# Optimization experiments

Measured on AMD Instinct MI355X. Metric: run time of the kernel, lower is better.

## Reference

```python
import jax, jax.numpy as jnp
import numpy as np
import math

G = 256      # graphs per batch
N0 = 256     # nodes per graph at input
RATIO = 0.5  # TopKPooling ratio


def gcn_conv(x, src, dst, ew, W, b):
    h = x @ W
    n = x.shape[0]
    deg = jnp.zeros((n,), x.dtype).at[dst].add(ew) + 1.0  # +1 for self-loop
    dinv = jax.lax.rsqrt(deg)
    norm = dinv[src] * dinv[dst] * ew
    agg = jnp.zeros_like(h).at[dst].add(norm[:, None] * h[src])
    return agg + h / deg[:, None] + b  # self-loop norm = 1/deg


def topk_pool(x, src, dst, ew, w, n_per_graph):
    # PyG TopKPooling: score = tanh(x.w/||w||); keep top ceil(ratio*n) per graph;
    # x_out = x[perm] * score[perm]; edges between dropped nodes are masked out.
    k = int(math.ceil(RATIO * n_per_graph))
    score = jnp.tanh((x @ w) / jnp.linalg.norm(w))
    top_s, top_i = jax.lax.top_k(score.reshape(G, n_per_graph), k)  # [G,k]
    perm = (top_i + (jnp.arange(G) * n_per_graph)[:, None]).reshape(-1)
    new_x = x[perm] * top_s.reshape(-1, 1)
    new_id = jnp.full((x.shape[0],), -1, jnp.int32).at[perm].set(
        jnp.arange(G * k, dtype=jnp.int32))
    ns, nd = new_id[src], new_id[dst]
    valid = (ns >= 0) & (nd >= 0)
    new_ew = ew * valid.astype(x.dtype)
    ns = jnp.where(valid, ns, 0)
    nd = jnp.where(valid, nd, 0)
    new_batch = jnp.repeat(jnp.arange(G, dtype=jnp.int32), k)
    return new_x, ns, nd, new_ew, new_batch, k


def readout(x, batch):
    # torch.cat([global_max_pool, global_mean_pool], dim=1)
    mx = jax.ops.segment_max(x, batch, num_segments=G)
    cnt = jax.ops.segment_sum(jnp.ones((x.shape[0],), x.dtype), batch, num_segments=G)
    mn = jax.ops.segment_sum(x, batch, num_segments=G) / cnt[:, None]
    return jnp.concatenate([mx, mn], axis=1)


def _forward(x, edge_index, batch, gcn_w0, gcn_b0, gcn_w1, gcn_b1, gcn_w2, gcn_b2,
             pool_w0, pool_w1, pool_w2, lin1_w, lin1_b, lin2_w, lin2_b, lin3_w, lin3_b):
    src, dst = edge_index[0], edge_index[1]
    ew = jnp.ones((src.shape[0],), x.dtype)
    npg = N0
    h = jax.nn.relu(gcn_conv(x, src, dst, ew, gcn_w0, gcn_b0))
    h, src, dst, ew, batch, npg = topk_pool(h, src, dst, ew, pool_w0, npg)
    out = readout(h, batch)
    for Wg, bg, pw in ((gcn_w1, gcn_b1, pool_w1), (gcn_w2, gcn_b2, pool_w2)):
        h = jax.nn.relu(gcn_conv(h, src, dst, ew, Wg, bg))
        h, src, dst, ew, batch, npg = topk_pool(h, src, dst, ew, pw, npg)
        out = out + readout(h, batch)
    h1 = jax.nn.relu(out @ lin1_w + lin1_b)  # dropout = identity (eval mode)
    h2 = jax.nn.relu(h1 @ lin2_w + lin2_b)
    logits = h2 @ lin3_w + lin3_b
    return jax.nn.log_softmax(logits, axis=-1)


def setup_inputs() -> dict:
    key = jax.random.key(0)
    ks = jax.random.split(key, 16)
    EPG = 2048  # edges per graph (avg degree 8)
    F_IN, H = 128, 256
    num_nodes, E = G * N0, G * EPG
    x = jax.random.normal(ks[0], (num_nodes, F_IN), jnp.float32)
    offs = jnp.repeat(jnp.arange(G, dtype=jnp.int32) * N0, EPG)
    src = offs + jax.random.randint(ks[1], (E,), 0, N0, dtype=jnp.int32)
    dst = offs + jax.random.randint(ks[2], (E,), 0, N0, dtype=jnp.int32)

    def glorot(k, shape):
        lim = float(np.sqrt(6.0 / (shape[0] + shape[1])))
        return jax.random.uniform(k, shape, jnp.float32, -lim, lim)

    return {
        "x": x,
        "edge_index": jnp.stack([src, dst]),
        "batch": jnp.arange(num_nodes, dtype=jnp.int32) // N0,
        "gcn_w0": glorot(ks[3], (F_IN, H)), "gcn_b0": jnp.zeros((H,), jnp.float32),
        "gcn_w1": glorot(ks[4], (H, H)), "gcn_b1": jnp.zeros((H,), jnp.float32),
        "gcn_w2": glorot(ks[5], (H, H)), "gcn_b2": jnp.zeros((H,), jnp.float32),
        "pool_w0": jax.random.normal(ks[6], (H,), jnp.float32) * 0.1,
        "pool_w1": jax.random.normal(ks[7], (H,), jnp.float32) * 0.1,
        "pool_w2": jax.random.normal(ks[8], (H,), jnp.float32) * 0.1,
        "lin1_w": glorot(ks[9], (2 * H, H)), "lin1_b": jnp.zeros((H,), jnp.float32),
        "lin2_w": glorot(ks[10], (H, H // 2)), "lin2_b": jnp.zeros((H // 2,), jnp.float32),
        "lin3_w": glorot(ks[11], (H // 2, 2)), "lin3_b": jnp.zeros((2,), jnp.float32),
    }


def reference(x, edge_index, batch, gcn_w0, gcn_b0, gcn_w1, gcn_b1, gcn_w2, gcn_b2,
              pool_w0, pool_w1, pool_w2, lin1_w, lin1_b, lin2_w, lin2_b, lin3_w, lin3_b):
    return _forward(x, edge_index, batch, gcn_w0, gcn_b0, gcn_w1, gcn_b1, gcn_w2, gcn_b2,
                    pool_w0, pool_w1, pool_w2, lin1_w, lin1_b, lin2_w, lin2_b, lin3_w, lin3_b)
```

## Files before the change

kernel.cpp:

```cpp
#include <hip/hip_runtime.h>
#include <hip/hip_bf16.h>
#include <math.h>

#define G_GRAPHS 256
#define EPG 2048
#define E_TOT 524288
#define HF 256
#define FIN 128

__global__ void init_cur(int* __restrict__ cur) {
    int i = blockIdx.x * blockDim.x + threadIdx.x;
    if (i < G_GRAPHS * 256) cur[i] = i & 255;
}

template <int K>
__global__ __launch_bounds__(256, 4)
void gemm_v8(const float* __restrict__ A, const float* __restrict__ W,
             float* __restrict__ C) {
    __shared__ __align__(16) float As[32 * 68];
    __shared__ __align__(16) float Wa[32 * 68];
    __shared__ __align__(16) float Wb[32 * 68];
    const int tid = threadIdx.x;
    const int tx = tid & 15;
    const int ty = tid >> 4;
    const int r0 = blockIdx.x * 64;
    const int c0 = blockIdx.y * 128;
    const int l8 = tid >> 3;
    const int kq = tid & 7;
    const int wkk = tid >> 5;
    const int wc = tid & 31;
    float acc[4][8] = {{0.f}};
    float4 va0, va1, vw0, vw1, vw2, vw3;

    auto load_regs = [&](int k0) {
        va0 = *(const float4*)&A[(size_t)(r0 + l8) * K + k0 + 4 * kq];
        va1 = *(const float4*)&A[(size_t)(r0 + 32 + l8) * K + k0 + 4 * kq];
        vw0 = *(const float4*)&W[(size_t)(k0 + 0  + wkk) * 256 + c0 + 4 * wc];
        vw1 = *(const float4*)&W[(size_t)(k0 + 8  + wkk) * 256 + c0 + 4 * wc];
        vw2 = *(const float4*)&W[(size_t)(k0 + 16 + wkk) * 256 + c0 + 4 * wc];
        vw3 = *(const float4*)&W[(size_t)(k0 + 24 + wkk) * 256 + c0 + 4 * wc];
    };
    auto write_stage = [&]() {
        {
            int rs = l8 ^ (kq << 3);
            As[(4 * kq + 0) * 68 + rs] = va0.x;
            As[(4 * kq + 1) * 68 + rs] = va0.y;
            As[(4 * kq + 2) * 68 + rs] = va0.z;
            As[(4 * kq + 3) * 68 + rs] = va0.w;
        }
        {
            int rs = (32 + l8) ^ (kq << 3);
            As[(4 * kq + 0) * 68 + rs] = va1.x;
            As[(4 * kq + 1) * 68 + rs] = va1.y;
            As[(4 * kq + 2) * 68 + rs] = va1.z;
            As[(4 * kq + 3) * 68 + rs] = va1.w;
        }
        if (wc < 16) {
            *(float4*)&Wa[(0  + wkk) * 68 + 4 * wc] = vw0;
            *(float4*)&Wa[(8  + wkk) * 68 + 4 * wc] = vw1;
            *(float4*)&Wa[(16 + wkk) * 68 + 4 * wc] = vw2;
            *(float4*)&Wa[(24 + wkk) * 68 + 4 * wc] = vw3;
        } else {
            *(float4*)&Wb[(0  + wkk) * 68 + 4 * (wc - 16)] = vw0;
            *(float4*)&Wb[(8  + wkk) * 68 + 4 * (wc - 16)] = vw1;
            *(float4*)&Wb[(16 + wkk) * 68 + 4 * (wc - 16)] = vw2;
            *(float4*)&Wb[(24 + wkk) * 68 + 4 * (wc - 16)] = vw3;
        }
    };
    auto compute = [&]() {
#pragma unroll 4
        for (int kk = 0; kk < 32; ++kk) {
            const int g = (ty * 4) ^ ((kk >> 2) << 3);
            const float4 a0 = *(const float4*)&As[kk * 68 + g];
            const float4 w0 = *(const float4*)&Wa[kk * 68 + tx * 4];
            const float4 w1 = *(const float4*)&Wb[kk * 68 + tx * 4];
            float av[4] = {a0.x, a0.y, a0.z, a0.w};
            float wv_[8] = {w0.x, w0.y, w0.z, w0.w, w1.x, w1.y, w1.z, w1.w};
#pragma unroll
            for (int i = 0; i < 4; ++i)
#pragma unroll
                for (int j = 0; j < 8; ++j)
                    acc[i][j] += av[i] * wv_[j];
        }
    };

    load_regs(0);
    write_stage();
    __syncthreads();
    for (int k0 = 0; k0 < K - 32; k0 += 32) {
        load_regs(k0 + 32);
        compute();
        __syncthreads();
        write_stage();
        __syncthreads();
    }
    compute();

#pragma unroll
    for (int i = 0; i < 4; ++i) {
        float4 v0 = make_float4(acc[i][0], acc[i][1], acc[i][2], acc[i][3]);
        float4 v1 = make_float4(acc[i][4], acc[i][5], acc[i][6], acc[i][7]);
        size_t base = (size_t)(r0 + ty * 4 + i) * 256 + c0 + tx * 4;
        *(float4*)&C[base] = v0;
        *(float4*)&C[base + 64] = v1;
    }
}

__global__ __launch_bounds__(256)
void csr_build(const int* __restrict__ ei, const int* __restrict__ cur, int npg,
               int* __restrict__ degS, float* __restrict__ dinvS,
               int* __restrict__ startsS, int2* __restrict__ slots2) {
    __shared__ int cul[EPG];
    __shared__ short dstv[EPG];
    __shared__ unsigned char rnk[EPG];
    __shared__ int h[32][256];
    __shared__ int cnt[256];
    __shared__ int st[256];
    const int g = blockIdx.x;
    const int t = threadIdx.x;
    const int lane = t & 63;
    const int wv = t >> 6;

    for (int i = t; i < 32 * 256; i += 256) ((int*)h)[i] = 0;
    for (int e = t; e < EPG; e += 256) {
        size_t idx = (size_t)g * EPG + e;
        int cu = cur[g * 256 + (ei[idx] - g * 256)];
        int cv = cur[g * 256 + (ei[E_TOT + idx] - g * 256)];
        bool valid = (cu >= 0 && cv >= 0);
        cul[e] = cu;
        dstv[e] = valid ? (short)cv : (short)256;
    }
    __syncthreads();
    for (int c = wv; c < 32; c += 4) {
        int e = c * 64 + lane;
        int d = (int)dstv[e];
        unsigned long long m = ~0ULL;
#pragma unroll
        for (int b = 0; b < 9; ++b) {
            unsigned long long bb = __ballot((d >> b) & 1);
            m &= ((d >> b) & 1) ? bb : ~bb;
        }
        int r = __popcll(m & ((1ULL << lane) - 1ULL));
        rnk[e] = (unsigned char)r;
        if (r == 0 && d < 256) h[c][d] = __popcll(m);
    }
    __syncthreads();
    if (t < npg) {
        int run = 0;
        for (int c = 0; c < 32; ++c) { int v = h[c][t]; h[c][t] = run; run += v; }
        cnt[t] = run;
        degS[g * npg + t] = run + 1;
        dinvS[g * npg + t] = 1.0f / sqrtf((float)(run + 1));
    }
    __syncthreads();
    if (t == 0) {
        int run = 0;
        for (int i = 0; i < npg; ++i) { st[i] = run; run += cnt[i]; }
    }
    __syncthreads();
    if (t < npg) startsS[g * npg + t] = g * EPG + st[t];
    for (int e = t; e < EPG; e += 256) {
        int d = (int)dstv[e];
        if (d < npg) {
            int slot = st[d] + h[e >> 6][d] + (int)rnk[e];
            int cu = cul[e];
            float dv = 1.0f / sqrtf((float)(cnt[cu] + 1));
            slots2[g * EPG + slot] = make_int2(g * npg + cu, __float_as_int(dv));
        }
    }
}

__global__ __launch_bounds__(256)
void agg_score2(const int* __restrict__ degS, const float* __restrict__ dinvS,
                const int* __restrict__ startsS, const int2* __restrict__ slots2,
                const float* __restrict__ HL, float* __restrict__ H2,
                const float* __restrict__ bias, const float* __restrict__ pw,
                float* __restrict__ score, int nbOver8) {
    __shared__ float vrow[4][256];
    const int t = threadIdx.x;
    const int wv = t >> 6;
    const int lane = t & 63;
    const int blk = (blockIdx.x & 7) * nbOver8 + (blockIdx.x >> 3);
    const int node = blk * 4 + wv;
    const int cntE = degS[node] - 1;
    const float degF = (float)(cntE + 1);
    const float dn = dinvS[node];
    const int2* sl = slots2 + startsS[node];
    float ax = 0.f, ay = 0.f, az = 0.f, aw = 0.f;
    int j = 0;
    for (; j + 8 <= cntE; j += 8) {
        int2 s[8];
#pragma unroll
        for (int u = 0; u < 8; ++u) s[u] = sl[j + u];
        float4 hv[8];
#pragma unroll
        for (int u = 0; u < 8; ++u)
            hv[u] = *(const float4*)&HL[(size_t)s[u].x * 256 + 4 * lane];
#pragma unroll
        for (int u = 0; u < 8; ++u) {
            float dv = __int_as_float(s[u].y);
            ax += dv * hv[u].x; ay += dv * hv[u].y;
            az += dv * hv[u].z; aw += dv * hv[u].w;
        }
    }
    for (; j + 4 <= cntE; j += 4) {
        int2 s[4];
#pragma unroll
        for (int u = 0; u < 4; ++u) s[u] = sl[j + u];
        float4 hv[4];
#pragma unroll
        for (int u = 0; u < 4; ++u)
            hv[u] = *(const float4*)&HL[(size_t)s[u].x * 256 + 4 * lane];
#pragma unroll
        for (int u = 0; u < 4; ++u) {
            float dv = __int_as_float(s[u].y);
            ax += dv * hv[u].x; ay += dv * hv[u].y;
            az += dv * hv[u].z; aw += dv * hv[u].w;
        }
    }
    for (; j < cntE; ++j) {
        int2 sv = sl[j];
        float dv = __int_as_float(sv.y);
        float4 hv = *(const float4*)&HL[(size_t)sv.x * 256 + 4 * lane];
        ax += dv * hv.x; ay += dv * hv.y; az += dv * hv.z; aw += dv * hv.w;
    }
    const float4 hn = *(const float4*)&HL[(size_t)node * 256 + 4 * lane];
    const float4 bi = *(const float4*)&bias[4 * lane];
    float4 v;
    v.x = ax * dn + hn.x / degF + bi.x;  v.x = fmaxf(v.x, 0.f);
    v.y = ay * dn + hn.y / degF + bi.y;  v.y = fmaxf(v.y, 0.f);
    v.z = az * dn + hn.z / degF + bi.z;  v.z = fmaxf(v.z, 0.f);
    v.w = aw * dn + hn.w / degF + bi.w;  v.w = fmaxf(v.w, 0.f);
    *(float4*)&H2[(size_t)node * 256 + 4 * lane] = v;
    *(float4*)&vrow[wv][4 * lane] = v;
    float pr = 0.f, s2p = 0.f;
    for (int jj = 0; jj < 4; ++jj) {
        int f = lane + 64 * jj;
        float w = pw[f];
        pr += vrow[wv][f] * w;
        s2p += w * w;
    }
    for (int off = 32; off; off >>= 1) {
        pr += __shfl_down(pr, off, 64);
        s2p += __shfl_down(s2p, off, 64);
    }
    s2p = __shfl(s2p, 0, 64);
    if (lane == 0) score[node] = tanhf(pr / sqrtf(s2p));
}

__global__ __launch_bounds__(256)
void topk_fused(const float* __restrict__ score, int npg, int k,
                const float* __restrict__ H2, float* __restrict__ OUT,
                float* __restrict__ outacc, int* __restrict__ cur, int first) {
    __shared__ float ss[256];
    __shared__ int si_[256];
    __shared__ int rankOf[256];
    const int g = blockIdx.x;
    const int t = threadIdx.x;
    if (t < npg) { ss[t] = score[g * npg + t]; si_[t] = t; }
    else         { ss[t] = -INFINITY; si_[t] = 0x7FFFFFFF; }
    for (int size = 2; size <= 256; size <<= 1) {
        for (int stride = size >> 1; stride > 0; stride >>= 1) {
            __syncthreads();
            int i = t, j = t ^ stride;
            if (j > i) {
                float a = ss[i], b = ss[j];
                int ia = si_[i], ib = si_[j];
                bool inOrder = (a > b) || (a == b && ia < ib);
                bool desc = ((i & size) == 0);
                if (desc ? !inOrder : inOrder) {
                    ss[i] = b; ss[j] = a; si_[i] = ib; si_[j] = ia;
                }
            }
        }
    }
    __syncthreads();
    rankOf[t] = -1;
    __syncthreads();
    if (t < k) rankOf[si_[t]] = t;
    __syncthreads();
    {
        int v = g * 256 + t;
        int c = cur[v];
        cur[v] = (c >= 0) ? rankOf[c] : -1;
    }
    const size_t gb = (size_t)g * npg * 256;
    float mx = -INFINITY, sm = 0.f;
    for (int n = 0; n < k; n += 4) {
        float v0 = H2[gb + (size_t)si_[n + 0] * 256 + t] * ss[n + 0];
        float v1 = H2[gb + (size_t)si_[n + 1] * 256 + t] * ss[n + 1];
        float v2 = H2[gb + (size_t)si_[n + 2] * 256 + t] * ss[n + 2];
        float v3 = H2[gb + (size_t)si_[n + 3] * 256 + t] * ss[n + 3];
        size_t ob = ((size_t)g * k + n) * 256 + t;
        OUT[ob]       = v0;
        OUT[ob + 256] = v1;
        OUT[ob + 512] = v2;
        OUT[ob + 768] = v3;
        mx = fmaxf(mx, v0); sm += v0;
        mx = fmaxf(mx, v1); sm += v1;
        mx = fmaxf(mx, v2); sm += v2;
        mx = fmaxf(mx, v3); sm += v3;
    }
    float mean = sm / (float)k;
    if (first) {
        outacc[g * 512 + t] = mx;
        outacc[g * 512 + 256 + t] = mean;
    } else {
        outacc[g * 512 + t] += mx;
        outacc[g * 512 + 256 + t] += mean;
    }
}

__global__ __launch_bounds__(256)
void mlp_head(const float* __restrict__ outacc,
              const float* __restrict__ l1w, const float* __restrict__ l1b,
              const float* __restrict__ l2w, const float* __restrict__ l2b,
              const float* __restrict__ l3w, const float* __restrict__ l3b,
              float* __restrict__ out) {
    __shared__ float row[512];
    __shared__ float h1[256];
    __shared__ float h2[128];
    const int g = blockIdx.x;
    const int t = threadIdx.x;
    row[t] = outacc[g * 512 + t];
    row[256 + t] = outacc[g * 512 + 256 + t];
    __syncthreads();
    {
        float a = l1b[t];
        for (int j = 0; j < 512; ++j) a += row[j] * l1w[j * 256 + t];
        h1[t] = fmaxf(a, 0.f);
    }
    __syncthreads();
    if (t < 128) {
        float a2 = l2b[t];
        for (int j = 0; j < 256; ++j) a2 += h1[j] * l2w[j * 128 + t];
        h2[t] = fmaxf(a2, 0.f);
    }
    __syncthreads();
    if (t == 0) {
        float l0 = l3b[0], l1 = l3b[1];
        for (int j = 0; j < 128; ++j) {
            float h = h2[j];
            l0 += h * l3w[j * 2 + 0];
            l1 += h * l3w[j * 2 + 1];
        }
        float m = fmaxf(l0, l1);
        float lse = m + logf(expf(l0 - m) + expf(l1 - m));
        out[g * 2 + 0] = l0 - lse;
        out[g * 2 + 1] = l1 - lse;
    }
}

__global__ __launch_bounds__(256, 1)
void gnn_mono(const float* __restrict__ x, const int* __restrict__ ei,
              const float* __restrict__ gw0, const float* __restrict__ gb0,
              const float* __restrict__ gw1, const float* __restrict__ gb1,
              const float* __restrict__ gw2, const float* __restrict__ gb2,
              const float* __restrict__ pw0, const float* __restrict__ pw1,
              const float* __restrict__ pw2,
              const float* __restrict__ l1w, const float* __restrict__ l1b,
              const float* __restrict__ l2w, const float* __restrict__ l2b,
              const float* __restrict__ l3w, const float* __restrict__ l3b,
              float* __restrict__ out, float* __restrict__ ws) {
    const int g = blockIdx.x;
    const int t = threadIdx.x;
    float* P = ws + (size_t)g * HF * 256;
    float* Q = ws + (size_t)G_GRAPHS * HF * 256 + (size_t)g * HF * 256;
    __shared__ int   eb[EPG];
    __shared__ int   slots[EPG];
    __shared__ int   curID[256];
    __shared__ int   cntL[256];
    __shared__ int   startL[256];
    __shared__ float degF[256];
    __shared__ float dinv[256];
    __shared__ float sa[256];
    __shared__ float ss[256];
    __shared__ int   si_[256];
    __shared__ float scoreV[256];
    __shared__ int   kept[128];
    __shared__ int   rankOf[256];
    __shared__ float row[512];
    for (int e = t; e < EPG; e += 256) {
        size_t idx = (size_t)g * EPG + e;
        eb[e] = ((ei[idx] - g * 256) << 8) | (ei[E_TOT + idx] - g * 256);
    }
    curID[t] = t;
    float accMx = 0.f, accMn = 0.f;
    const float* GW[3] = {gw0, gw1, gw2};
    const float* GB[3] = {gb0, gb1, gb2};
    const float* PW[3] = {pw0, pw1, pw2};
    const int kk[3] = {128, 64, 32};
    int npg = 256;
    __syncthreads();
    for (int s = 0; s < 3; ++s) {
        const int knext = kk[s];
        {
            const float* Wp = GW[s];
            const int K = (s == 0) ? FIN : HF;
            for (int n = 0; n < npg; ++n) {
                if (s == 0) { if (t < FIN) sa[t] = x[(size_t)(g * 256 + n) * FIN + t]; }
                else sa[t] = P[(size_t)n * HF + t];
                __syncthreads();
                float a = 0.f;
                for (int k2 = 0; k2 < K; ++k2) a += sa[k2] * Wp[k2 * HF + t];
                Q[(size_t)n * HF + t] = a;
                __syncthreads();
            }
        }
        cntL[t] = 0;
        __syncthreads();
        for (int e = t; e < EPG; e += 256) {
            int p = eb[e];
            int cu = curID[p >> 8], cv = curID[p & 255];
            if (cu >= 0 && cv >= 0) atomicAdd(&cntL[cv], 1);
        }
        __syncthreads();
        if (t == 0) { int run = 0; for (int i = 0; i < npg; ++i) { startL[i] = run; run += cntL[i]; } }
        __syncthreads();
        if (t < npg) {
            float d = (float)cntL[t] + 1.0f;
            degF[t] = d;
            dinv[t] = 1.0f / sqrtf(d);
            int c = startL[t];
            for (int e = 0; e < EPG; ++e) {
                int p = eb[e];
                int cu = curID[p >> 8], cv = curID[p & 255];
                if (cu >= 0 && cv >= 0 && cv == t) slots[c++] = e;
            }
        }
        __syncthreads();
        {
            const float bb = GB[s][t];
            for (int n = 0; n < npg; ++n) {
                float acc = 0.f;
                const int s0 = startL[n], s1 = s0 + cntL[n];
                for (int j = s0; j < s1; ++j) {
                    int scur = curID[eb[slots[j]] >> 8];
                    acc += dinv[scur] * Q[(size_t)scur * HF + t];
                }
                float v = acc * dinv[n] + Q[(size_t)n * HF + t] / degF[n] + bb;
                P[(size_t)n * HF + t] = fmaxf(v, 0.f);
            }
        }
        __syncthreads();
        {
            const float* pwp = PW[s];
            const int lane = t & 63, wv = t >> 6;
            float s2p = 0.f;
            for (int j = 0; j < 4; ++j) { float w = pwp[lane + 64 * j]; s2p += w * w; }
            for (int off = 32; off; off >>= 1) s2p += __shfl_down(s2p, off, 64);
            s2p = __shfl(s2p, 0, 64);
            const float nw = sqrtf(s2p);
            for (int n = wv; n < npg; n += 4) {
                float pr = 0.f;
                for (int j = 0; j < 4; ++j) { int f = lane + 64 * j; pr += P[(size_t)n * HF + f] * pwp[f]; }
                for (int off = 32; off; off >>= 1) pr += __shfl_down(pr, off, 64);
                if (lane == 0) scoreV[n] = tanhf(pr / nw);
            }
        }
        __syncthreads();
        if (t < npg) { ss[t] = scoreV[t]; si_[t] = t; }
        else         { ss[t] = -INFINITY; si_[t] = 0x7FFFFFFF; }
        for (int size = 2; size <= 256; size <<= 1) {
            for (int stride = size >> 1; stride > 0; stride >>= 1) {
                __syncthreads();
                int i = t, j = t ^ stride;
                if (j > i) {
                    float a = ss[i], b = ss[j];
                    int ia = si_[i], ib = si_[j];
                    bool inOrder = (a > b) || (a == b && ia < ib);
                    bool desc = ((i & size) == 0);
                    if (desc ? !inOrder : inOrder) { ss[i] = b; ss[j] = a; si_[i] = ib; si_[j] = ia; }
                }
            }
        }
        __syncthreads();
        if (t < knext) kept[t] = si_[t];
        __syncthreads();
        {
            float mx = -INFINITY, sm = 0.f;
            for (int n = 0; n < knext; ++n) {
                int o = kept[n];
                float vv = P[(size_t)o * HF + t] * scoreV[o];
                Q[(size_t)n * HF + t] = vv;
                mx = fmaxf(mx, vv);
                sm += vv;
            }
            accMx += mx;
            accMn += sm / (float)knext;
        }
        rankOf[t] = -1;
        __syncthreads();
        if (t < knext) rankOf[kept[t]] = t;
        __syncthreads();
        { int c = curID[t]; curID[t] = (c >= 0) ? rankOf[c] : -1; }
        __syncthreads();
        { float* tmp = P; P = Q; Q = tmp; }
        npg = knext;
    }
    row[t] = accMx;
    row[256 + t] = accMn;
    __syncthreads();
    { float a = l1b[t]; for (int j = 0; j < 512; ++j) a += row[j] * l1w[j * 256 + t]; scoreV[t] = fmaxf(a, 0.f); }
    __syncthreads();
    if (t < 128) { float a2 = l2b[t]; for (int j = 0; j < 256; ++j) a2 += scoreV[j] * l2w[j * 128 + t]; sa[t] = fmaxf(a2, 0.f); }
    __syncthreads();
    if (t == 0) {
        float l0 = l3b[0], l1 = l3b[1];
        for (int j = 0; j < 128; ++j) { float h = sa[j]; l0 += h * l3w[j * 2 + 0]; l1 += h * l3w[j * 2 + 1]; }
        float m = fmaxf(l0, l1);
        float lse = m + logf(expf(l0 - m) + expf(l1 - m));
        out[g * 2 + 0] = l0 - lse;
        out[g * 2 + 1] = l1 - lse;
    }
}

extern "C" void kernel_launch(void* const* d_in, const int* in_sizes, int n_in,
                              void* d_out, int out_size, void* d_ws, size_t ws_size,
                              hipStream_t stream) {
    const float* x   = (const float*)d_in[0];
    const int*   ei  = (const int*)d_in[1];
    const float* gw0 = (const float*)d_in[3];
    const float* gb0 = (const float*)d_in[4];
    const float* gw1 = (const float*)d_in[5];
    const float* gb1 = (const float*)d_in[6];
    const float* gw2 = (const float*)d_in[7];
    const float* gb2 = (const float*)d_in[8];
    const float* pw0 = (const float*)d_in[9];
    const float* pw1 = (const float*)d_in[10];
    const float* pw2 = (const float*)d_in[11];
    const float* l1w = (const float*)d_in[12];
    const float* l1b = (const float*)d_in[13];
    const float* l2w = (const float*)d_in[14];
    const float* l2b = (const float*)d_in[15];
    const float* l3w = (const float*)d_in[16];
    const float* l3b = (const float*)d_in[17];
    float* out = (float*)d_out;

    const size_t SLAB = (size_t)65536 * 256;
    char* p = (char*)d_ws;
    float* P      = (float*)p; p += SLAB * 4;
    float* Q      = (float*)p; p += SLAB * 4;
    int*   cur    = (int*)p;   p += (size_t)65536 * 4;
    int*   degS   = (int*)p;   p += (size_t)65536 * 4;
    float* dinvS  = (float*)p; p += (size_t)65536 * 4;
    int*   starts = (int*)p;   p += (size_t)65536 * 4;
    int2*  slots2 = (int2*)p;  p += (size_t)E_TOT * 8;
    float* score  = (float*)p; p += (size_t)65536 * 4;
    int*   kept   = (int*)p;   p += (size_t)32768 * 4;
    float* outacc = (float*)p; p += (size_t)G_GRAPHS * 512 * 4;
    const size_t needed = (size_t)(p - (char*)d_ws);

    if (ws_size < needed) {
        gnn_mono<<<G_GRAPHS, 256, 0, stream>>>(
            x, ei, gw0, gb0, gw1, gb1, gw2, gb2, pw0, pw1, pw2,
            l1w, l1b, l2w, l2b, l3w, l3b, out, (float*)d_ws);
        return;
    }

    init_cur<<<(G_GRAPHS * 256 + 255) / 256, 256, 0, stream>>>(cur);

    const int   npg[3] = {256, 128, 64};
    const int   kk[3]  = {128, 64, 32};
    const int   Ns[3]  = {65536, 32768, 16384};
    const float* GW[3] = {gw0, gw1, gw2};
    const float* GB[3] = {gb0, gb1, gb2};
    const float* PW[3] = {pw0, pw1, pw2};

    float* HLs[3]   = {P, Q, P};
    float* H2s[3]   = {Q, P, Q};
    float* POOLs[3] = {P, Q, P};

    for (int s = 0; s < 3; ++s) {
        const int n = Ns[s];
        const int k = kk[s];
        if (s == 0) {
            gemm_v8<FIN><<<dim3(n / 64, 2), 256, 0, stream>>>(x, GW[s], HLs[s]);
        } else {
            gemm_v8<HF><<<dim3(n / 64, 2), 256, 0, stream>>>(POOLs[s - 1], GW[s], HLs[s]);
        }
        csr_build<<<G_GRAPHS, 256, 0, stream>>>(ei, cur, npg[s],
                                                degS, dinvS, starts, slots2);
        agg_score2<<<n / 4, 256, 0, stream>>>(degS, dinvS, starts, slots2,
                                              HLs[s], H2s[s], GB[s], PW[s], score,
                                              n / 32);
        topk_fused<<<G_GRAPHS, 256, 0, stream>>>(score, npg[s], k,
                                                 H2s[s], POOLs[s], outacc, cur,
                                                 s == 0 ? 1 : 0);
    }

    mlp_head<<<G_GRAPHS, 256, 0, stream>>>(outacc, l1w, l1b, l2w, l2b, l3w, l3b, out);
}
```

Baseline: 456.3 us.

## Fuse CSR build into topk and init kernels, fold final topk into MLP head

```diff
diff --git a/kernel.cpp b/kernel.cpp
--- a/kernel.cpp
+++ b/kernel.cpp
@@ -7,11 +7,6 @@
 #define E_TOT 524288
 #define HF 256
 #define FIN 128
-
-__global__ void init_cur(int* __restrict__ cur) {
-    int i = blockIdx.x * blockDim.x + threadIdx.x;
-    if (i < G_GRAPHS * 256) cur[i] = i & 255;
-}
 
 template <int K>
 __global__ __launch_bounds__(256, 4)
@@ -106,10 +101,70 @@
     }
 }
 
+template <bool IDENT>
+__device__ __forceinline__ void csr_body(
+    const int* __restrict__ ei, int g, int t, int npg, const int* curL,
+    int* __restrict__ degS, float* __restrict__ dinvS,
+    int* __restrict__ startsS, int2* __restrict__ slots2,
+    int* cul, short* dstv, unsigned char* rnk, int (*h)[256],
+    int* cnt, int* st) {
+    const int lane = t & 63;
+    const int wv = t >> 6;
+    for (int i = t; i < 32 * 256; i += 256) ((int*)h)[i] = 0;
+    for (int e = t; e < EPG; e += 256) {
+        size_t idx = (size_t)g * EPG + e;
+        int u = ei[idx] - g * 256;
+        int v = ei[E_TOT + idx] - g * 256;
+        int cu = IDENT ? u : curL[u];
+        int cv = IDENT ? v : curL[v];
+        bool valid = (cu >= 0 && cv >= 0);
+        cul[e] = cu;
+        dstv[e] = valid ? (short)cv : (short)256;
+    }
+    __syncthreads();
+    for (int c = wv; c < 32; c += 4) {
+        int e = c * 64 + lane;
+        int d = (int)dstv[e];
+        unsigned long long m = ~0ULL;
+#pragma unroll
+        for (int b = 0; b < 9; ++b) {
+            unsigned long long bb = __ballot((d >> b) & 1);
+            m &= ((d >> b) & 1) ? bb : ~bb;
+        }
+        int r = __popcll(m & ((1ULL << lane) - 1ULL));
+        rnk[e] = (unsigned char)r;
+        if (r == 0 && d < 256) h[c][d] = __popcll(m);
+    }
+    __syncthreads();
+    if (t < npg) {
+        int run = 0;
+        for (int c = 0; c < 32; ++c) { int v = h[c][t]; h[c][t] = run; run += v; }
+        cnt[t] = run;
+        degS[g * npg + t] = run + 1;
+        dinvS[g * npg + t] = 1.0f / sqrtf((float)(run + 1));
+    }
+    __syncthreads();
+    if (t == 0) {
+        int run = 0;
+        for (int i = 0; i < npg; ++i) { st[i] = run; run += cnt[i]; }
+    }
+    __syncthreads();
+    if (t < npg) startsS[g * npg + t] = g * EPG + st[t];
+    for (int e = t; e < EPG; e += 256) {
+        int d = (int)dstv[e];
+        if (d < npg) {
+            int slot = st[d] + h[e >> 6][d] + (int)rnk[e];
+            int cu = cul[e];
+            float dv = 1.0f / sqrtf((float)(cnt[cu] + 1));
+            slots2[g * EPG + slot] = make_int2(g * npg + cu, __float_as_int(dv));
+        }
+    }
+}
+
 __global__ __launch_bounds__(256)
-void csr_build(const int* __restrict__ ei, const int* __restrict__ cur, int npg,
-               int* __restrict__ degS, float* __restrict__ dinvS,
-               int* __restrict__ startsS, int2* __restrict__ slots2) {
+void fused_init_csr(const int* __restrict__ ei, int* __restrict__ cur,
+                    int* __restrict__ degS, float* __restrict__ dinvS,
+                    int* __restrict__ startsS, int2* __restrict__ slots2) {
     __shared__ int cul[EPG];
     __shared__ short dstv[EPG];
     __shared__ unsigned char rnk[EPG];
@@ -118,56 +173,9 @@
     __shared__ int st[256];
     const int g = blockIdx.x;
     const int t = threadIdx.x;
-    const int lane = t & 63;
-    const int wv = t >> 6;
-
-    for (int i = t; i < 32 * 256; i += 256) ((int*)h)[i] = 0;
-    for (int e = t; e < EPG; e += 256) {
-        size_t idx = (size_t)g * EPG + e;
-        int cu = cur[g * 256 + (ei[idx] - g * 256)];
-        int cv = cur[g * 256 + (ei[E_TOT + idx] - g * 256)];
-        bool valid = (cu >= 0 && cv >= 0);
-        cul[e] = cu;
-        dstv[e] = valid ? (short)cv : (short)256;
-    }
-    __syncthreads();
-    for (int c = wv; c < 32; c += 4) {
-        int e = c * 64 + lane;
-        int d = (int)dstv[e];
-        unsigned long long m = ~0ULL;
-#pragma unroll
-        for (int b = 0; b < 9; ++b) {
-            unsigned long long bb = __ballot((d >> b) & 1);
-            m &= ((d >> b) & 1) ? bb : ~bb;
-        }
-        int r = __popcll(m & ((1ULL << lane) - 1ULL));
-        rnk[e] = (unsigned char)r;
-        if (r == 0 && d < 256) h[c][d] = __popcll(m);
-    }
-    __syncthreads();
-    if (t < npg) {
-        int run = 0;
-        for (int c = 0; c < 32; ++c) { int v = h[c][t]; h[c][t] = run; run += v; }
-        cnt[t] = run;
-        degS[g * npg + t] = run + 1;
-        dinvS[g * npg + t] = 1.0f / sqrtf((float)(run + 1));
-    }
-    __syncthreads();
-    if (t == 0) {
-        int run = 0;
-        for (int i = 0; i < npg; ++i) { st[i] = run; run += cnt[i]; }
-    }
-    __syncthreads();
-    if (t < npg) startsS[g * npg + t] = g * EPG + st[t];
-    for (int e = t; e < EPG; e += 256) {
-        int d = (int)dstv[e];
-        if (d < npg) {
-            int slot = st[d] + h[e >> 6][d] + (int)rnk[e];
-            int cu = cul[e];
-            float dv = 1.0f / sqrtf((float)(cnt[cu] + 1));
-            slots2[g * EPG + slot] = make_int2(g * npg + cu, __float_as_int(dv));
-        }
-    }
+    cur[g * 256 + t] = t;
+    csr_body<true>(ei, g, t, 256, nullptr, degS, dinvS, startsS, slots2,
+                   cul, dstv, rnk, h, cnt, st);
 }
 
 __global__ __launch_bounds__(256)
@@ -249,12 +257,22 @@
 }
 
 __global__ __launch_bounds__(256)
-void topk_fused(const float* __restrict__ score, int npg, int k,
-                const float* __restrict__ H2, float* __restrict__ OUT,
-                float* __restrict__ outacc, int* __restrict__ cur, int first) {
+void fused_topk_csr(const float* __restrict__ score, int npg, int k,
+                    const float* __restrict__ H2, float* __restrict__ OUT,
+                    float* __restrict__ outacc, int* __restrict__ cur, int first,
+                    const int* __restrict__ ei,
+                    int* __restrict__ degS, float* __restrict__ dinvS,
+                    int* __restrict__ startsS, int2* __restrict__ slots2) {
     __shared__ float ss[256];
     __shared__ int si_[256];
     __shared__ int rankOf[256];
+    __shared__ int curL[256];
+    __shared__ int cul[EPG];
+    __shared__ short dstv[EPG];
+    __shared__ unsigned char rnk[EPG];
+    __shared__ int h[32][256];
+    __shared__ int cnt[256];
+    __shared__ int st[256];
     const int g = blockIdx.x;
     const int t = threadIdx.x;
     if (t < npg) { ss[t] = score[g * npg + t]; si_[t] = t; }
@@ -282,7 +300,9 @@
     {
         int v = g * 256 + t;
         int c = cur[v];
-        cur[v] = (c >= 0) ? rankOf[c] : -1;
+        int nc = (c >= 0) ? rankOf[c] : -1;
+        cur[v] = nc;
+        curL[t] = nc;
     }
     const size_t gb = (size_t)g * npg * 256;
     float mx = -INFINITY, sm = 0.f;
@@ -309,21 +329,59 @@
         outacc[g * 512 + t] += mx;
         outacc[g * 512 + 256 + t] += mean;
     }
+    __syncthreads();
+    csr_body<false>(ei, g, t, k, curL, degS, dinvS, startsS, slots2,
+                    cul, dstv, rnk, h, cnt, st);
 }
 
 __global__ __launch_bounds__(256)
-void mlp_head(const float* __restrict__ outacc,
-              const float* __restrict__ l1w, const float* __restrict__ l1b,
-              const float* __restrict__ l2w, const float* __restrict__ l2b,
-              const float* __restrict__ l3w, const float* __restrict__ l3b,
-              float* __restrict__ out) {
+void fused_topk_mlp(const float* __restrict__ score, int npg, int k,
+                    const float* __restrict__ H2,
+                    const float* __restrict__ outacc,
+                    const float* __restrict__ l1w, const float* __restrict__ l1b,
+                    const float* __restrict__ l2w, const float* __restrict__ l2b,
+                    const float* __restrict__ l3w, const float* __restrict__ l3b,
+                    float* __restrict__ out) {
+    __shared__ float ss[256];
+    __shared__ int si_[256];
     __shared__ float row[512];
     __shared__ float h1[256];
     __shared__ float h2[128];
     const int g = blockIdx.x;
     const int t = threadIdx.x;
-    row[t] = outacc[g * 512 + t];
-    row[256 + t] = outacc[g * 512 + 256 + t];
+    if (t < npg) { ss[t] = score[g * npg + t]; si_[t] = t; }
+    else         { ss[t] = -INFINITY; si_[t] = 0x7FFFFFFF; }
+    for (int size = 2; size <= 256; size <<= 1) {
+        for (int stride = size >> 1; stride > 0; stride >>= 1) {
+            __syncthreads();
+            int i = t, j = t ^ stride;
+            if (j > i) {
+                float a = ss[i], b = ss[j];
+                int ia = si_[i], ib = si_[j];
+                bool inOrder = (a > b) || (a == b && ia < ib);
+                bool desc = ((i & size) == 0);
+                if (desc ? !inOrder : inOrder) {
+                    ss[i] = b; ss[j] = a; si_[i] = ib; si_[j] = ia;
+                }
+            }
+        }
+    }
+    __syncthreads();
+    const size_t gb = (size_t)g * npg * 256;
+    float mx = -INFINITY, sm = 0.f;
+    for (int n = 0; n < k; n += 4) {
+        float v0 = H2[gb + (size_t)si_[n + 0] * 256 + t] * ss[n + 0];
+        float v1 = H2[gb + (size_t)si_[n + 1] * 256 + t] * ss[n + 1];
+        float v2 = H2[gb + (size_t)si_[n + 2] * 256 + t] * ss[n + 2];
+        float v3 = H2[gb + (size_t)si_[n + 3] * 256 + t] * ss[n + 3];
+        mx = fmaxf(mx, v0); sm += v0;
+        mx = fmaxf(mx, v1); sm += v1;
+        mx = fmaxf(mx, v2); sm += v2;
+        mx = fmaxf(mx, v3); sm += v3;
+    }
+    float mean = sm / (float)k;
+    row[t]       = outacc[g * 512 + t] + mx;
+    row[256 + t] = outacc[g * 512 + 256 + t] + mean;
     __syncthreads();
     {
         float a = l1b[t];
@@ -558,8 +616,6 @@
         return;
     }
 
-    init_cur<<<(G_GRAPHS * 256 + 255) / 256, 256, 0, stream>>>(cur);
-
     const int   npg[3] = {256, 128, 64};
     const int   kk[3]  = {128, 64, 32};
     const int   Ns[3]  = {65536, 32768, 16384};
@@ -570,6 +626,9 @@
     float* HLs[3]   = {P, Q, P};
     float* H2s[3]   = {Q, P, Q};
     float* POOLs[3] = {P, Q, P};
+
+    fused_init_csr<<<G_GRAPHS, 256, 0, stream>>>(ei, cur, degS, dinvS,
+                                                 starts, slots2);
 
     for (int s = 0; s < 3; ++s) {
         const int n = Ns[s];
@@ -579,15 +638,17 @@
         } else {
             gemm_v8<HF><<<dim3(n / 64, 2), 256, 0, stream>>>(POOLs[s - 1], GW[s], HLs[s]);
         }
-        csr_build<<<G_GRAPHS, 256, 0, stream>>>(ei, cur, npg[s],
-                                                degS, dinvS, starts, slots2);
         agg_score2<<<n / 4, 256, 0, stream>>>(degS, dinvS, starts, slots2,
                                               HLs[s], H2s[s], GB[s], PW[s], score,
                                               n / 32);
-        topk_fused<<<G_GRAPHS, 256, 0, stream>>>(score, npg[s], k,
-                                                 H2s[s], POOLs[s], outacc, cur,
-                                                 s == 0 ? 1 : 0);
-    }
-
-    mlp_head<<<G_GRAPHS, 256, 0, stream>>>(outacc, l1w, l1b, l2w, l2b, l3w, l3b, out);
-}
+        if (s < 2) {
+            fused_topk_csr<<<G_GRAPHS, 256, 0, stream>>>(
+                score, npg[s], k, H2s[s], POOLs[s], outacc, cur, s == 0 ? 1 : 0,
+                ei, degS, dinvS, starts, slots2);
+        } else {
+            fused_topk_mlp<<<G_GRAPHS, 256, 0, stream>>>(
+                score, npg[s], k, H2s[s], outacc,
+                l1w, l1b, l2w, l2b, l3w, l3b, out);
+        }
+    }
+}
```

New measurement: 444.0 us. -2.7%, faster.
